# Kernel optimization log

Hardware: AMD Instinct MI355X
Metric: run time of the kernel (lower is better)

The kernel has to match this reference:

```python
import jax, jax.numpy as jnp
import numpy as np
import math

D = 1024
B, S = 4, 2048


def setup_inputs() -> dict:
    key = jax.random.key(0)
    ks = jax.random.split(key, 16)
    sc = 0.02
    def lin(k, dout, din):
        kw, kb = jax.random.split(k)
        return (sc * jax.random.normal(kw, (dout, din), jnp.float32),
                sc * jax.random.normal(kb, (dout,), jnp.float32))
    Wq, bq = lin(ks[0], D, D)
    Wk, bk = lin(ks[1], D, D)
    Wv, bv = lin(ks[2], D, D)
    Wmu, bmu = lin(ks[3], D, D)
    Wlv, blv = lin(ks[4], D, D)
    Wg, bg = lin(ks[5], 1, D)
    gamma = jnp.ones((D,), jnp.float32)
    beta = jnp.zeros((D,), jnp.float32)
    x = jax.random.normal(ks[6], (B, S, D), jnp.float32)
    eps = jax.random.normal(ks[7], (B, S, D), jnp.float32)
    return dict(x=x, eps=eps, Wq=Wq, bq=bq, Wk=Wk, bk=bk, Wv=Wv, bv=bv,
                Wmu=Wmu, bmu=bmu, Wlv=Wlv, blv=blv, Wg=Wg, bg=bg,
                gamma=gamma, beta=beta)


def _layernorm(x, gamma, beta, eps=1e-5):
    mu = jnp.mean(x, axis=-1, keepdims=True)
    var = jnp.mean(jnp.square(x - mu), axis=-1, keepdims=True)
    return (x - mu) * jax.lax.rsqrt(var + eps) * gamma + beta


def reference(x, eps, Wq, bq, Wk, bk, Wv, bv, Wmu, bmu, Wlv, blv, Wg, bg, gamma, beta):
    d = x.shape[-1]
    Q = jnp.einsum('bsd,ed->bse', x, Wq) + bq
    K = jnp.einsum('bsd,ed->bse', x, Wk) + bk
    V = jnp.einsum('bsd,ed->bse', x, Wv) + bv
    scores = jnp.einsum('bqd,bkd->bqk', Q, K) / (math.sqrt(d) * 1.5)
    attn = jax.nn.softmax(scores, axis=-1)
    h = jnp.einsum('bqk,bkd->bqd', attn, V)
    mu = jnp.einsum('bsd,ed->bse', h, Wmu) + bmu
    logvar = jnp.einsum('bsd,ed->bse', h, Wlv) + blv
    std = jnp.exp(0.5 * logvar)
    z = jax.nn.relu(mu + eps * std)
    p_gate = jax.nn.sigmoid(jnp.einsum('bd,ed->be', h.mean(axis=1), Wg) + bg)
    out = _layernorm(x + z, gamma, beta)
    return out, mu, logvar, p_gate.squeeze(-1)
```

## Files before the change

kernel.cpp:

```cpp
#include <hip/hip_runtime.h>

typedef unsigned short u16;
typedef __attribute__((ext_vector_type(8))) short bf16x8;
typedef __attribute__((ext_vector_type(4))) float f32x4;

__device__ inline float bf2f(u16 h) {
    union { unsigned u; float f; } v; v.u = ((unsigned)h) << 16; return v.f;
}
__device__ inline u16 f2bf(float f) {
    union { float f; unsigned u; } v; v.f = f;
    unsigned r = v.u + 0x7fffu + ((v.u >> 16) & 1u);
    return (u16)(r >> 16);
}

__device__ inline void gl_lds16(const u16* g, u16* l) {
    __builtin_amdgcn_global_load_lds(
        (const __attribute__((address_space(1))) void*)g,
        (__attribute__((address_space(3))) void*)l, 16, 0, 0);
}

__device__ __forceinline__ void wgbar() {
    asm volatile("" ::: "memory");
    __builtin_amdgcn_s_barrier();
    asm volatile("" ::: "memory");
}
#define VMW(n) asm volatile("s_waitcnt vmcnt(" #n ")" ::: "memory")

__global__ __launch_bounds__(256) void cvt_bf16_k(
    const float* __restrict__ s0, u16* __restrict__ d0, long long n0,
    const float* __restrict__ s1, u16* __restrict__ d1, long long n1,
    const float* __restrict__ s2, u16* __restrict__ d2, long long n2,
    const float* __restrict__ s3, u16* __restrict__ d3, long long n3)
{
    int y = blockIdx.y;
    const float* s = (y == 0) ? s0 : (y == 1) ? s1 : (y == 2) ? s2 : s3;
    u16* d         = (y == 0) ? d0 : (y == 1) ? d1 : (y == 2) ? d2 : d3;
    long long n    = (y == 0) ? n0 : (y == 1) ? n1 : (y == 2) ? n2 : n3;
    for (long long i = (long long)blockIdx.x * 256 + threadIdx.x; i < n;
         i += (long long)gridDim.x * 256) {
        float4 v = ((const float4*)s)[i];
        union { u16 h[4]; unsigned long long u; } p;
        p.h[0] = f2bf(v.x); p.h[1] = f2bf(v.y);
        p.h[2] = f2bf(v.z); p.h[3] = f2bf(v.w);
        ((unsigned long long*)d)[i] = p.u;
    }
}

#define STA(T, SL2, S)                                                        \
    { const u16* g_ = Ag + (long long)((S) * 64 + w * 8 + srow) * K           \
                      + (long long)(T) * 64 + scol;                           \
      gl_lds16(g_, &As[SL2][(S) * 4096 + w * 512]); }

#define STB(T, SL2, S)                                                        \
    { const u16* g_ = Bg + (long long)(bn0 + (S) * 64 + w * 8 + srow) * ldb   \
                      + (long long)(T) * 64 + scol;                           \
      gl_lds16(g_, &Bs[SL2][(S) * 4096 + w * 512]); }

template <int COUTF32, int BIASROW, int NSPLIT>
__global__ __launch_bounds__(512, 2) void gemm8(
    const u16* __restrict__ A, const u16* __restrict__ Bt,
    const float* __restrict__ bias0, const float* __restrict__ bias1,
    void* __restrict__ C0, void* __restrict__ C1,
    int M, int N, int K, int ldb, float scale,
    long long sAb, long long sBb, long long sCb, long long bofs_stride)
{
    __shared__ u16 As[3][8192];
    __shared__ u16 Bs[3][16384];

    int gx = gridDim.x, gy = gridDim.y;
    int n = gx * gy * gridDim.z;
    int flat = (blockIdx.z * gy + blockIdx.y) * gx + blockIdx.x;
    int L = (flat & 7) * (n >> 3) + (flat >> 3);
    int bz = L / (gx * gy);
    int rr = L - bz * gx * gy;
    int by = rr / gx, bx = rr - (rr / gx) * gx;

    int bm0 = bx * 128;
    int bn0 = by * 256;
    int b   = bz;
    int tid = threadIdx.x;
    int w = tid >> 6, l = tid & 63;
    int wm = w >> 2;
    int wn = w & 3;
    int lane15 = l & 15, quad = l >> 4;
    int xr = (l & 7) << 3;

    int srow = l >> 3;
    int scol = ((l & 7) ^ srow) * 8;

    const u16* Ag = A  + (long long)b * sAb + (long long)bm0 * K;
    const u16* Bg = Bt + (long long)b * sBb + (long long)(bm0 >> 11) * bofs_stride;

    f32x4 acc[4][4];
#pragma unroll
    for (int i = 0; i < 4; i++)
#pragma unroll
        for (int j = 0; j < 4; j++) acc[i][j] = (f32x4)(0.0f);

    int NT = K >> 6;

    STA(0, 0, 0); STA(0, 0, 1);
    STB(0, 0, 0); STB(0, 0, 1); STB(0, 0, 2); STB(0, 0, 3);
    STA(1, 1, 0); STA(1, 1, 1);
    STB(1, 1, 0); STB(1, 1, 1); STB(1, 1, 2); STB(1, 1, 3);
    VMW(6);
    wgbar();

    int sl = 0, sl2 = 2;
    for (int t = 0; t < NT; ++t) {
        bool pf = (t + 2 < NT);
        int t2 = t + 2;
        if (pf) {
            STA(t2, sl2, 0); STA(t2, sl2, 1);
            STB(t2, sl2, 0); STB(t2, sl2, 1);
            STB(t2, sl2, 2); STB(t2, sl2, 3);
        }
#pragma unroll
        for (int ks = 0; ks < 2; ks++) {
            bf16x8 av[4], bvv[4];
#pragma unroll
            for (int ii = 0; ii < 4; ii++)
                av[ii] = *(const bf16x8*)&As[sl][
                    ((wm * 64 + ii * 16 + lane15) * 64 + ks * 32 + quad * 8) ^ xr];
#pragma unroll
            for (int jj = 0; jj < 4; jj++)
                bvv[jj] = *(const bf16x8*)&Bs[sl][
                    ((wn * 64 + jj * 16 + lane15) * 64 + ks * 32 + quad * 8) ^ xr];
            __builtin_amdgcn_s_setprio(1);
#pragma unroll
            for (int ii = 0; ii < 4; ii++)
#pragma unroll
                for (int jj = 0; jj < 4; jj++)
                    acc[ii][jj] = __builtin_amdgcn_mfma_f32_16x16x32_bf16(
                        av[ii], bvv[jj], acc[ii][jj], 0, 0, 0);
            __builtin_amdgcn_s_setprio(0);
        }
        if (pf) { VMW(6); } else { VMW(0); }
        wgbar();
        sl  = (sl  == 2) ? 0 : sl + 1;
        sl2 = (sl2 == 2) ? 0 : sl2 + 1;
    }

    float rowb_[4][4];
    if (BIASROW) {
#pragma unroll
        for (int i = 0; i < 4; i++)
#pragma unroll
            for (int r = 0; r < 4; r++)
                rowb_[i][r] = bias0[bm0 + wm * 64 + i * 16 + quad * 4 + r];
    }
#pragma unroll
    for (int jj = 0; jj < 4; jj++) {
        int col = bn0 + wn * 64 + jj * 16 + lane15;
        int seg, cl, cstride;
        if (NSPLIT == 1) { seg = 0; cl = col; cstride = N; }
        else             { seg = col >> 10; cl = col & 1023; cstride = 1024; }
        const float* bp = (seg == 0) ? bias0 : bias1;
        void* cb = (seg == 0) ? C0 : C1;
        u16*   c16 = (u16*)cb   + (long long)b * sCb;
        float* c32 = (float*)cb + (long long)b * sCb;
        float bvc = (!BIASROW && bp) ? bp[cl] : 0.0f;
#pragma unroll
        for (int i = 0; i < 4; i++) {
            int row0 = bm0 + wm * 64 + i * 16 + quad * 4;
#pragma unroll
            for (int r = 0; r < 4; r++) {
                float v = acc[i][jj][r] * scale + (BIASROW ? rowb_[i][r] : bvc);
                if (COUTF32) c32[(long long)(row0 + r) * cstride + cl] = v;
                else         c16[(long long)(row0 + r) * cstride + cl] = f2bf(v);
            }
        }
    }
}

__global__ __launch_bounds__(256) void softmax_k(u16* __restrict__ Sc)
{
    long long row = blockIdx.x;
    u16* s = Sc + row * 2048;
    int t = threadIdx.x;

    uint4 raw = *(const uint4*)(s + t * 8);
    const u16* rp = (const u16*)&raw;
    float v[8];
    float mx = -3.4e38f;
#pragma unroll
    for (int j = 0; j < 8; j++) { v[j] = bf2f(rp[j]); mx = fmaxf(mx, v[j]); }
#pragma unroll
    for (int o = 32; o > 0; o >>= 1) mx = fmaxf(mx, __shfl_xor(mx, o));
    __shared__ float redm[4];
    if ((t & 63) == 0) redm[t >> 6] = mx;
    __syncthreads();
    mx = fmaxf(fmaxf(redm[0], redm[1]), fmaxf(redm[2], redm[3]));

    float sum = 0.0f;
#pragma unroll
    for (int j = 0; j < 8; j++) { v[j] = __expf(v[j] - mx); sum += v[j]; }
#pragma unroll
    for (int o = 32; o > 0; o >>= 1) sum += __shfl_xor(sum, o);
    __shared__ float reds[4];
    if ((t & 63) == 0) reds[t >> 6] = sum;
    __syncthreads();
    sum = reds[0] + reds[1] + reds[2] + reds[3];

    float inv = 1.0f / sum;
    u16 o8[8];
#pragma unroll
    for (int j = 0; j < 8; j++) o8[j] = f2bf(v[j] * inv);
    *(uint4*)(s + t * 8) = *(const uint4*)o8;
}

__global__ __launch_bounds__(256) void gate_partial(const u16* __restrict__ h,
                                                    const float* __restrict__ Wg,
                                                    float* __restrict__ part)
{
    int b = blockIdx.x, c = blockIdx.y;
    int t = threadIdx.x;
    int tx = t & 127;
    int ty = t >> 7;
    int d0 = tx * 8;
    const u16* hb = h + (long long)b * 2048 * 1024 + (long long)c * 16 * 1024;

    float wg[8];
#pragma unroll
    for (int j = 0; j < 8; j++) wg[j] = Wg[d0 + j];

    float acc = 0.0f;
    for (int s = ty; s < 16; s += 2) {
        bf16x8 hv = *(const bf16x8*)&hb[(long long)s * 1024 + d0];
        const u16* hp = (const u16*)&hv;
#pragma unroll
        for (int j = 0; j < 8; j++) acc += bf2f(hp[j]) * wg[j];
    }
#pragma unroll
    for (int o = 32; o > 0; o >>= 1) acc += __shfl_xor(acc, o);
    __shared__ float red[4];
    if ((t & 63) == 0) red[t >> 6] = acc;
    __syncthreads();
    if (t == 0) part[b * 128 + c] = red[0] + red[1] + red[2] + red[3];
}

__global__ void gate_final(const float* __restrict__ part,
                           const float* __restrict__ bg, float* __restrict__ outp)
{
    int t = threadIdx.x;
    if (t < 4) {
        float s = 0.0f;
        for (int c = 0; c < 128; c++) s += part[t * 128 + c];
        float v = s * (1.0f / 2048.0f) + bg[0];
        outp[t] = 1.0f / (1.0f + __expf(-v));
    }
}

__global__ __launch_bounds__(256) void epilogue_k(
    const float* __restrict__ x, const float* __restrict__ ep,
    const float* __restrict__ mu, const float* __restrict__ lv,
    const float* __restrict__ gamma, const float* __restrict__ beta,
    float* __restrict__ out)
{
    long long base = (long long)blockIdx.x * 1024;
    int t = threadIdx.x;
    float y[4];
    float sum = 0.0f, sq = 0.0f;
#pragma unroll
    for (int j = 0; j < 4; j++) {
        int i = j * 256 + t;
        float xv = x[base + i];
        float ev = ep[base + i];
        float m  = mu[base + i];
        float sd = __expf(0.5f * lv[base + i]);
        float z  = fmaxf(m + ev * sd, 0.0f);
        float yy = xv + z;
        y[j] = yy; sum += yy; sq += yy * yy;
    }
#pragma unroll
    for (int o = 32; o > 0; o >>= 1) { sum += __shfl_xor(sum, o); sq += __shfl_xor(sq, o); }
    __shared__ float rs[4], rq[4];
    if ((t & 63) == 0) { rs[t >> 6] = sum; rq[t >> 6] = sq; }
    __syncthreads();
    sum = rs[0] + rs[1] + rs[2] + rs[3];
    sq  = rq[0] + rq[1] + rq[2] + rq[3];
    float mean = sum * (1.0f / 1024.0f);
    float var  = fmaxf(sq * (1.0f / 1024.0f) - mean * mean, 0.0f);
    float rstd = rsqrtf(var + 1e-5f);
#pragma unroll
    for (int j = 0; j < 4; j++) {
        int i = j * 256 + t;
        out[base + i] = (y[j] - mean) * rstd * gamma[i] + beta[i];
    }
}

extern "C" void kernel_launch(void* const* d_in, const int* in_sizes, int n_in,
                              void* d_out, int out_size, void* d_ws, size_t ws_size,
                              hipStream_t stream)
{
    const float* x     = (const float*)d_in[0];
    const float* ep    = (const float*)d_in[1];
    const float* Wq    = (const float*)d_in[2];
    const float* bq    = (const float*)d_in[3];
    const float* Wk    = (const float*)d_in[4];
    const float* bk    = (const float*)d_in[5];
    const float* Wv    = (const float*)d_in[6];
    const float* bv    = (const float*)d_in[7];
    const float* Wmu   = (const float*)d_in[8];
    const float* bmu   = (const float*)d_in[9];
    const float* Wlv   = (const float*)d_in[10];
    const float* blv   = (const float*)d_in[11];
    const float* Wg    = (const float*)d_in[12];
    const float* bg    = (const float*)d_in[13];
    const float* gamma = (const float*)d_in[14];
    const float* beta  = (const float*)d_in[15];
    float* out = (float*)d_out;

    const int M = 8192;
    const int D = 1024;
    const int S = 2048;

    float* mu_out = out + 8388608LL;
    float* lv_out = out + 16777216LL;
    float* pg_out = out + 25165824LL;

    u16* xb   = (u16*)out;
    u16* Wqb  = (u16*)out + 8388608LL;
    u16* Wkb  = (u16*)out + 9437184LL;
    u16* Wvb  = (u16*)out + 10485760LL;
    u16* Sc   = (u16*)out;
    u16* Q    = (u16*)mu_out;
    u16* Kb   = (u16*)mu_out + 8388608LL;
    u16* Vt   = (u16*)lv_out;
    u16* h    = (u16*)d_ws;
    float* part = (float*)out;
    u16* Wmub = (u16*)out + 2097152LL;
    u16* Wlvb = (u16*)out + 3145728LL;

    dim3 blk(256), blk8(512);

    cvt_bf16_k<<<dim3(2048, 4), blk, 0, stream>>>(
        x,  xb,  2097152LL,
        Wq, Wqb, 262144LL,
        Wk, Wkb, 262144LL,
        Wv, Wvb, 262144LL);

    gemm8<0, 0, 2><<<dim3(64, 8, 1), blk8, 0, stream>>>(
        xb, Wqb, bq, bk, Q, Kb,
        M, 2048, D, D, 1.0f, 0, 0, 0, 0);

    gemm8<0, 1, 1><<<dim3(8, 32, 1), blk8, 0, stream>>>(
        Wvb, xb, bv, nullptr, Vt, nullptr,
        D, 8192, D, D, 1.0f, 0, 0, 0, 0);

    gemm8<0, 0, 1><<<dim3(16, 8, 4), blk8, 0, stream>>>(
        Q, Kb, nullptr, nullptr, Sc, nullptr,
        S, S, D, D, 1.0f / 48.0f,
        (long long)S * D, (long long)S * D, (long long)S * S, 0);

    softmax_k<<<dim3(8192), blk, 0, stream>>>(Sc);

    gemm8<0, 0, 1><<<dim3(64, 4, 1), blk8, 0, stream>>>(
        Sc, Vt, nullptr, nullptr, h, nullptr,
        M, D, S, 8192, 1.0f, 0, 0, 0, 2048);

    cvt_bf16_k<<<dim3(512, 2), blk, 0, stream>>>(
        Wmu, Wmub, 262144LL,
        Wlv, Wlvb, 262144LL,
        nullptr, nullptr, 0LL,
        nullptr, nullptr, 0LL);

    gemm8<1, 0, 2><<<dim3(64, 8, 1), blk8, 0, stream>>>(
        h, Wmub, bmu, blv, (void*)mu_out, (void*)lv_out,
        M, 2048, D, D, 1.0f, 0, 0, 0, 0);

    gate_partial<<<dim3(4, 128), blk, 0, stream>>>(h, Wg, part);
    gate_final<<<dim3(1), dim3(64), 0, stream>>>(part, bg, pg_out);

    epilogue_k<<<dim3(8192), blk, 0, stream>>>(x, ep, mu_out, lv_out, gamma, beta, out);
}
```

Measured before the change: 461.2 us.

## Enlarge GEMM tile to 256x256 with double-buffered, interleaved load/MFMA pipeline

Replaces the 128x256 triple-buffered GEMM with a 256x256 tile per workgroup, using a 2-stage LDS buffer split into halves. Each K-step is broken into four MFMA quadrants, with the global-to-LDS loads for the next tile spread between them under extra barriers. The larger tile raises arithmetic intensity and halves the grid size. In exchange it doubles accumulator registers and adds more barriers per iteration, which may hurt occupancy or leave too few blocks to fill the CUs on the smaller GEMMs.

```diff
diff --git a/kernel.cpp b/kernel.cpp
--- a/kernel.cpp
+++ b/kernel.cpp
@@ -46,26 +46,36 @@
     }
 }
 
-#define STA(T, SL2, S)                                                        \
-    { const u16* g_ = Ag + (long long)((S) * 64 + w * 8 + srow) * K           \
+#define STA_S(T, H, SI)                                                       \
+    { const u16* g_ = Ag + (long long)((H) * 128 + (SI) * 64 + w * 8 + srow)  \
+                      * K + (long long)(T) * 64 + scol;                       \
+      gl_lds16(g_, &As[(T) & 1][H][(SI) * 4096 + w * 512]); }
+
+#define STB_S(T, NQ)                                                          \
+    { const u16* g_ = Bg + (long long)(bn0 + (NQ) * 64 + w * 8 + srow) * ldb  \
                       + (long long)(T) * 64 + scol;                           \
-      gl_lds16(g_, &As[SL2][(S) * 4096 + w * 512]); }
-
-#define STB(T, SL2, S)                                                        \
-    { const u16* g_ = Bg + (long long)(bn0 + (S) * 64 + w * 8 + srow) * ldb   \
-                      + (long long)(T) * 64 + scol;                           \
-      gl_lds16(g_, &Bs[SL2][(S) * 4096 + w * 512]); }
+      gl_lds16(g_, &Bs[(T) & 1][(NQ) >> 1][((NQ) & 1) * 4096 + w * 512]); }
+
+#define MMA16(AV, BV, I0)                                                     \
+    __builtin_amdgcn_s_setprio(1);                                            \
+    _Pragma("unroll")                                                         \
+    for (int ii = 0; ii < 4; ii++)                                            \
+        _Pragma("unroll")                                                     \
+        for (int jj = 0; jj < 4; jj++)                                        \
+            acc[(I0) + ii][jj] = __builtin_amdgcn_mfma_f32_16x16x32_bf16(     \
+                AV[ii], BV[jj], acc[(I0) + ii][jj], 0, 0, 0);                 \
+    __builtin_amdgcn_s_setprio(0);
 
 template <int COUTF32, int BIASROW, int NSPLIT>
-__global__ __launch_bounds__(512, 2) void gemm8(
+__global__ __launch_bounds__(512, 2) void gemm256(
     const u16* __restrict__ A, const u16* __restrict__ Bt,
     const float* __restrict__ bias0, const float* __restrict__ bias1,
     void* __restrict__ C0, void* __restrict__ C1,
     int M, int N, int K, int ldb, float scale,
     long long sAb, long long sBb, long long sCb, long long bofs_stride)
 {
-    __shared__ u16 As[3][8192];
-    __shared__ u16 Bs[3][16384];
+    __shared__ u16 As[2][2][8192];
+    __shared__ u16 Bs[2][2][8192];
 
     int gx = gridDim.x, gy = gridDim.y;
     int n = gx * gy * gridDim.z;
@@ -75,7 +85,7 @@
     int rr = L - bz * gx * gy;
     int by = rr / gx, bx = rr - (rr / gx) * gx;
 
-    int bm0 = bx * 128;
+    int bm0 = bx * 256;
     int bn0 = by * 256;
     int b   = bz;
     int tid = threadIdx.x;
@@ -91,63 +101,83 @@
     const u16* Ag = A  + (long long)b * sAb + (long long)bm0 * K;
     const u16* Bg = Bt + (long long)b * sBb + (long long)(bm0 >> 11) * bofs_stride;
 
-    f32x4 acc[4][4];
-#pragma unroll
-    for (int i = 0; i < 4; i++)
+    f32x4 acc[8][4];
+#pragma unroll
+    for (int i = 0; i < 8; i++)
 #pragma unroll
         for (int j = 0; j < 4; j++) acc[i][j] = (f32x4)(0.0f);
 
     int NT = K >> 6;
 
-    STA(0, 0, 0); STA(0, 0, 1);
-    STB(0, 0, 0); STB(0, 0, 1); STB(0, 0, 2); STB(0, 0, 3);
-    STA(1, 1, 0); STA(1, 1, 1);
-    STB(1, 1, 0); STB(1, 1, 1); STB(1, 1, 2); STB(1, 1, 3);
-    VMW(6);
+    STA_S(0, 0, 0); STA_S(0, 1, 0);
+    STB_S(0, 0); STB_S(0, 1); STB_S(0, 2); STB_S(0, 3);
+    STA_S(0, 0, 1); STA_S(0, 1, 1);
+    STA_S(1, 0, 0); STA_S(1, 1, 0);
+    STB_S(1, 0); STB_S(1, 1); STB_S(1, 2); STB_S(1, 3);
+    VMW(8);
     wgbar();
 
-    int sl = 0, sl2 = 2;
     for (int t = 0; t < NT; ++t) {
-        bool pf = (t + 2 < NT);
-        int t2 = t + 2;
-        if (pf) {
-            STA(t2, sl2, 0); STA(t2, sl2, 1);
-            STB(t2, sl2, 0); STB(t2, sl2, 1);
-            STB(t2, sl2, 2); STB(t2, sl2, 3);
+        int T = t + 1;
+        int s = t & 1;
+        bool sf = (t > 0) && (T < NT);
+        bool st = (T < NT);
+        const u16* Ah = &As[s][wm][0];
+        const u16* Bh = &Bs[s][wn >> 1][0];
+        int brow = (wn & 1) * 64;
+
+        bf16x8 a0[4], a1[4], b0[4], b1[4];
+#pragma unroll
+        for (int ii = 0; ii < 4; ii++) {
+            int r = ii * 16 + lane15;
+            a0[ii] = *(const bf16x8*)&Ah[(r * 64 + quad * 8) ^ xr];
+            a1[ii] = *(const bf16x8*)&Ah[(r * 64 + 32 + quad * 8) ^ xr];
         }
 #pragma unroll
-        for (int ks = 0; ks < 2; ks++) {
-            bf16x8 av[4], bvv[4];
-#pragma unroll
-            for (int ii = 0; ii < 4; ii++)
-                av[ii] = *(const bf16x8*)&As[sl][
-                    ((wm * 64 + ii * 16 + lane15) * 64 + ks * 32 + quad * 8) ^ xr];
-#pragma unroll
-            for (int jj = 0; jj < 4; jj++)
-                bvv[jj] = *(const bf16x8*)&Bs[sl][
-                    ((wn * 64 + jj * 16 + lane15) * 64 + ks * 32 + quad * 8) ^ xr];
-            __builtin_amdgcn_s_setprio(1);
-#pragma unroll
-            for (int ii = 0; ii < 4; ii++)
-#pragma unroll
-                for (int jj = 0; jj < 4; jj++)
-                    acc[ii][jj] = __builtin_amdgcn_mfma_f32_16x16x32_bf16(
-                        av[ii], bvv[jj], acc[ii][jj], 0, 0, 0);
-            __builtin_amdgcn_s_setprio(0);
+        for (int jj = 0; jj < 4; jj++) {
+            int r = brow + jj * 16 + lane15;
+            b0[jj] = *(const bf16x8*)&Bh[(r * 64 + quad * 8) ^ xr];
         }
-        if (pf) { VMW(6); } else { VMW(0); }
-        wgbar();
-        sl  = (sl  == 2) ? 0 : sl + 1;
-        sl2 = (sl2 == 2) ? 0 : sl2 + 1;
-    }
-
-    float rowb_[4][4];
+        if (sf) { STA_S(T, 0, 0); STA_S(T, 1, 0); STB_S(T, 0); }
+        wgbar();
+        MMA16(a0, b0, 0);
+        wgbar();
+
+#pragma unroll
+        for (int jj = 0; jj < 4; jj++) {
+            int r = brow + jj * 16 + lane15;
+            b1[jj] = *(const bf16x8*)&Bh[(r * 64 + 32 + quad * 8) ^ xr];
+        }
+        if (sf) { STB_S(T, 1); STB_S(T, 2); STB_S(T, 3); }
+        if (t == NT - 1) { VMW(0); } else { VMW(6); }
+        wgbar();
+        MMA16(a1, b1, 0);
+        wgbar();
+
+#pragma unroll
+        for (int ii = 0; ii < 4; ii++) {
+            int r = 64 + ii * 16 + lane15;
+            a0[ii] = *(const bf16x8*)&Ah[(r * 64 + quad * 8) ^ xr];
+            a1[ii] = *(const bf16x8*)&Ah[(r * 64 + 32 + quad * 8) ^ xr];
+        }
+        if (st) { STA_S(T, 0, 1); }
+        wgbar();
+        MMA16(a0, b0, 4);
+        wgbar();
+
+        if (st) { STA_S(T, 1, 1); VMW(2); }
+        wgbar();
+        MMA16(a1, b1, 4);
+        wgbar();
+    }
+
+    float rowb_[8][4];
     if (BIASROW) {
 #pragma unroll
-        for (int i = 0; i < 4; i++)
+        for (int i = 0; i < 8; i++)
 #pragma unroll
             for (int r = 0; r < 4; r++)
-                rowb_[i][r] = bias0[bm0 + wm * 64 + i * 16 + quad * 4 + r];
+                rowb_[i][r] = bias0[bm0 + wm * 128 + i * 16 + quad * 4 + r];
     }
 #pragma unroll
     for (int jj = 0; jj < 4; jj++) {
@@ -161,8 +191,8 @@
         float* c32 = (float*)cb + (long long)b * sCb;
         float bvc = (!BIASROW && bp) ? bp[cl] : 0.0f;
 #pragma unroll
-        for (int i = 0; i < 4; i++) {
-            int row0 = bm0 + wm * 64 + i * 16 + quad * 4;
+        for (int i = 0; i < 8; i++) {
+            int row0 = bm0 + wm * 128 + i * 16 + quad * 4;
 #pragma unroll
             for (int r = 0; r < 4; r++) {
                 float v = acc[i][jj][r] * scale + (BIASROW ? rowb_[i][r] : bvc);
@@ -340,22 +370,22 @@
         Wk, Wkb, 262144LL,
         Wv, Wvb, 262144LL);
 
-    gemm8<0, 0, 2><<<dim3(64, 8, 1), blk8, 0, stream>>>(
+    gemm256<0, 0, 2><<<dim3(32, 8, 1), blk8, 0, stream>>>(
         xb, Wqb, bq, bk, Q, Kb,
         M, 2048, D, D, 1.0f, 0, 0, 0, 0);
 
-    gemm8<0, 1, 1><<<dim3(8, 32, 1), blk8, 0, stream>>>(
+    gemm256<0, 1, 1><<<dim3(4, 32, 1), blk8, 0, stream>>>(
         Wvb, xb, bv, nullptr, Vt, nullptr,
         D, 8192, D, D, 1.0f, 0, 0, 0, 0);
 
-    gemm8<0, 0, 1><<<dim3(16, 8, 4), blk8, 0, stream>>>(
+    gemm256<0, 0, 1><<<dim3(8, 8, 4), blk8, 0, stream>>>(
         Q, Kb, nullptr, nullptr, Sc, nullptr,
         S, S, D, D, 1.0f / 48.0f,
         (long long)S * D, (long long)S * D, (long long)S * S, 0);
 
     softmax_k<<<dim3(8192), blk, 0, stream>>>(Sc);
 
-    gemm8<0, 0, 1><<<dim3(64, 4, 1), blk8, 0, stream>>>(
+    gemm256<0, 0, 1><<<dim3(32, 4, 1), blk8, 0, stream>>>(
         Sc, Vt, nullptr, nullptr, h, nullptr,
         M, D, S, 8192, 1.0f, 0, 0, 0, 2048);
 
@@ -365,7 +395,7 @@
         nullptr, nullptr, 0LL,
         nullptr, nullptr, 0LL);
 
-    gemm8<1, 0, 2><<<dim3(64, 8, 1), blk8, 0, stream>>>(
+    gemm256<1, 0, 2><<<dim3(32, 8, 1), blk8, 0, stream>>>(
         h, Wmub, bmu, blv, (void*)mu_out, (void*)lv_out,
         M, 2048, D, D, 1.0f, 0, 0, 0, 0);
 
```

After: 512.4 us. 1.11x slower.
